# Kernel optimization log

Measured on AMD Instinct MI355X. Metric: run time of the kernel, lower is better.

The kernel has to match this reference:

```python
import jax, jax.numpy as jnp
import numpy as np

B, S, D, F, E, K = 2, 2048, 1024, 4096, 8, 2


def setup_inputs() -> dict:
    key = jax.random.key(0)
    ks = jax.random.split(key, 6)
    s = 0.02  # init scale
    return {
        "x": jax.random.normal(ks[0], (B, S, D), dtype=jnp.float32),
        "Wr": jax.random.normal(ks[1], (D, E), dtype=jnp.float32) * s,
        "br": jnp.zeros((E,), dtype=jnp.float32),
        "W1": jax.random.normal(ks[2], (E, D, F), dtype=jnp.float32) * s,
        "b1": jnp.zeros((E, F), dtype=jnp.float32),
        "W2": jax.random.normal(ks[3], (E, F, D), dtype=jnp.float32) * s,
        "b2": jnp.zeros((E, D), dtype=jnp.float32),
        "top_k": K,
    }


def reference(x, Wr, br, W1, b1, W2, b2, top_k):
    b, s, d = x.shape
    e = Wr.shape[1]
    xt = x.reshape(-1, d)                              # [T, D], T = b*s
    logits = xt @ Wr + br                              # [T, E]
    probs = jax.nn.softmax(logits, axis=-1)            # [T, E] router probabilities
    topw, topi = jax.lax.top_k(probs, top_k)           # [T, K] each
    # combine weight per (token, expert): weight if expert in token's top-k else 0
    cw = jnp.sum(jax.nn.one_hot(topi, e, dtype=x.dtype) * topw[..., None], axis=1)  # [T, E]
    # dense grouped FFN: every expert over every token, then weighted combine
    h = jax.nn.relu(jnp.einsum('td,edf->tef', xt, W1) + b1)   # [T, E, F]
    y = jnp.einsum('tef,efd->ted', h, W2) + b2                # [T, E, D]
    out = jnp.einsum('te,ted->td', cw, y).reshape(b, s, d)    # [B, S, D]
    return out, probs.reshape(b, s, e)
```

## Files before the change

kernel.cpp:

```cpp
#include <hip/hip_runtime.h>
#include <hip/hip_bf16.h>


#define T_TOK 4096
#define D_DIM 1024
#define F_DIM 4096
#define E_NUM 8
#define CAP_ROWS 9216
#define N_TILES (CAP_ROWS/128)

typedef __attribute__((ext_vector_type(8))) short short8v;
typedef __attribute__((ext_vector_type(8))) unsigned short ushort8v;
typedef __attribute__((ext_vector_type(4))) float f32x4;

static __device__ __forceinline__ unsigned short f2bf(float f){
  union { float f; unsigned u; } v; v.f = f;
  unsigned r = (v.u + 0x7fffu + ((v.u >> 16) & 1u)) >> 16;
  return (unsigned short)r;
}
static __device__ __forceinline__ float bf2f(unsigned short s){
  union { unsigned u; float f; } v; v.u = ((unsigned)s) << 16;
  return v.f;
}

static __device__ __forceinline__ void gload16(const void* g, void* l) {
  __builtin_amdgcn_global_load_lds(
      (const __attribute__((address_space(1))) unsigned int*)g,
      (__attribute__((address_space(3))) unsigned int*)l, 16, 0, 0);
}

__global__ __launch_bounds__(256) void k_init(int* counts, int* cursor,
                                              int* rows_token, float* rows_w){
  const int gid = blockIdx.x * 256 + threadIdx.x;
  if (gid < E_NUM) counts[gid] = 0;
  else if (gid < 2*E_NUM) cursor[gid - E_NUM] = 0;
  if (gid < CAP_ROWS) { rows_token[gid] = 0; rows_w[gid] = 0.f; }
}

__global__ __launch_bounds__(256) void k_router(
    const float* __restrict__ x, const float* __restrict__ Wr,
    const float* __restrict__ br, float* __restrict__ probs_out,
    int* __restrict__ topi, float* __restrict__ topw, int* __restrict__ counts)
{
  const int lane = threadIdx.x & 63;
  const int t = blockIdx.x * 4 + (threadIdx.x >> 6);
  float xv[16];
  #pragma unroll
  for (int i = 0; i < 16; ++i) xv[i] = x[(size_t)t*D_DIM + i*64 + lane];
  float pe[E_NUM];
  #pragma unroll
  for (int e = 0; e < E_NUM; ++e) {
    float p = 0.f;
    #pragma unroll
    for (int i = 0; i < 16; ++i) p += xv[i] * Wr[(i*64 + lane)*E_NUM + e];
    #pragma unroll
    for (int off = 32; off >= 1; off >>= 1) p += __shfl_xor(p, off);
    pe[e] = p + br[e];
  }
  float m = pe[0];
  #pragma unroll
  for (int e = 1; e < E_NUM; ++e) m = fmaxf(m, pe[e]);
  float s = 0.f;
  #pragma unroll
  for (int e = 0; e < E_NUM; ++e) { pe[e] = expf(pe[e] - m); s += pe[e]; }
  const float inv = 1.f / s;
  int e1 = 0; float v1 = pe[0];
  #pragma unroll
  for (int e = 1; e < E_NUM; ++e) if (pe[e] > v1) { v1 = pe[e]; e1 = e; }
  int e2 = (e1 == 0) ? 1 : 0; float v2 = pe[e2];
  #pragma unroll
  for (int e = 0; e < E_NUM; ++e) if (e != e1 && pe[e] > v2) { v2 = pe[e]; e2 = e; }
  if (lane == 0) {
    #pragma unroll
    for (int e = 0; e < E_NUM; ++e) probs_out[(size_t)t*E_NUM + e] = pe[e] * inv;
    topi[t*2+0] = e1; topw[t*2+0] = v1 * inv;
    topi[t*2+1] = e2; topw[t*2+1] = v2 * inv;
    atomicAdd(&counts[e1], 1);
    atomicAdd(&counts[e2], 1);
  }
}

__global__ void k_scan(const int* __restrict__ counts, int* __restrict__ pbase,
                       int* __restrict__ tile_e)
{
  if (threadIdx.x == 0 && blockIdx.x == 0) {
    int base = 0;
    for (int e = 0; e < E_NUM; ++e) {
      pbase[e] = base;
      const int nt = (counts[e] + 127) >> 7;
      for (int i = 0; i < nt; ++i) tile_e[(base >> 7) + i] = e;
      base += nt << 7;
    }
    pbase[E_NUM] = base;
    for (int tt = base >> 7; tt < N_TILES; ++tt) tile_e[tt] = -1;
  }
}

__global__ __launch_bounds__(256) void k_assign(
    const int* __restrict__ topi, const float* __restrict__ topw,
    const int* __restrict__ pbase, int* __restrict__ cursor,
    int* __restrict__ rows_token, float* __restrict__ rows_w,
    int* __restrict__ pair_of)
{
  const int t = blockIdx.x * 256 + threadIdx.x;
  if (t < T_TOK) {
    #pragma unroll
    for (int k = 0; k < 2; ++k) {
      const int e = topi[t*2+k];
      const int slot = atomicAdd(&cursor[e], 1);
      const int pid = pbase[e] + slot;
      rows_token[pid] = t;
      rows_w[pid] = topw[t*2+k];
      pair_of[t*2+k] = pid;
    }
  }
}

__global__ __launch_bounds__(256) void k_cvt_x(const float* __restrict__ x,
                                               unsigned short* __restrict__ xbf)
{
  const int i = (blockIdx.x * 256 + threadIdx.x) * 4;
  const float4 v = *(const float4*)&x[i];
  ushort4 o; o.x=f2bf(v.x); o.y=f2bf(v.y); o.z=f2bf(v.z); o.w=f2bf(v.w);
  *(ushort4*)&xbf[i] = o;
}

template<int R, int C>
__global__ __launch_bounds__(256) void k_tcvt(const float* __restrict__ in,
                                              unsigned short* __restrict__ out)
{
  const size_t eo = (size_t)blockIdx.z * R * C;
  const int r0 = blockIdx.y * 64, c0 = blockIdx.x * 64;
  __shared__ unsigned short ls[64][66];
  const int t = threadIdx.x;
  const int rr = t >> 4, cc = (t & 15) * 4;
  #pragma unroll
  for (int p = 0; p < 4; ++p) {
    const float4 v = *(const float4*)&in[eo + (size_t)(r0 + p*16 + rr)*C + c0 + cc];
    ls[p*16+rr][cc+0]=f2bf(v.x); ls[p*16+rr][cc+1]=f2bf(v.y);
    ls[p*16+rr][cc+2]=f2bf(v.z); ls[p*16+rr][cc+3]=f2bf(v.w);
  }
  __syncthreads();
  const int kc = (t & 7) * 8, nn0 = t >> 3;
  #pragma unroll
  for (int p = 0; p < 2; ++p) {
    const int nn = nn0 + p*32;
    ushort8v o;
    #pragma unroll
    for (int j = 0; j < 8; ++j) o[j] = ls[kc + j][nn];
    *(ushort8v*)&out[eo + (size_t)(c0 + nn)*R + r0 + kc] = o;
  }
}

template<bool GATHER, int NDIM, int KDIM, bool EPI1>
__global__ __launch_bounds__(256, 2) void k_gemm(
    const unsigned short* __restrict__ A,
    const unsigned short* __restrict__ Bt,
    const float* __restrict__ bias,
    const int* __restrict__ tile_e,
    const int* __restrict__ rows_token,
    const float* __restrict__ rows_w,
    unsigned short* __restrict__ outp)
{
  const int e = tile_e[blockIdx.y];
  if (e < 0) return;
  const int rt = blockIdx.y * 128;
  const int ntc = blockIdx.x * 128;
  __shared__ __align__(16) unsigned short LB[3][2][128*32];
  const int tid = threadIdx.x;
  const int lane = tid & 63;
  const int w = tid >> 6;
  const int seg = w & 1;
  const int isB = (w >= 2) ? 1 : 0;
  const int lrow = lane >> 2, lchunk = lane & 3;
  const unsigned short* gsrc[4];
  unsigned lds_off[4];
  if (w < 2) {
    #pragma unroll
    for (int i = 0; i < 4; ++i) {
      const int rl = seg*64 + i*16 + lrow;
      const int rowidx = GATHER ? rows_token[rt + rl] : (rt + rl);
      gsrc[i] = A + (size_t)rowidx * KDIM + lchunk*8;
      lds_off[i] = (unsigned)((seg*64 + i*16)*32);
    }
  } else {
    const unsigned short* Be = Bt + (size_t)e * NDIM * KDIM;
    #pragma unroll
    for (int i = 0; i < 4; ++i) {
      const int rl = seg*64 + i*16 + lrow;
      gsrc[i] = Be + (size_t)(ntc + rl) * KDIM + lchunk*8;
      lds_off[i] = (unsigned)((seg*64 + i*16)*32);
    }
  }
  const int wr = w >> 1, wc = w & 1;
  const int cl = lane & 15, rgb = lane >> 4;
  f32x4 acc[4][4] = {};

  constexpr int NT = KDIM / 32;
  #pragma unroll
  for (int i = 0; i < 4; ++i) gload16(gsrc[i] + 0,  &LB[0][isB][lds_off[i]]);
  #pragma unroll
  for (int i = 0; i < 4; ++i) gload16(gsrc[i] + 32, &LB[1][isB][lds_off[i]]);
  asm volatile("s_waitcnt vmcnt(4)" ::: "memory");
  __builtin_amdgcn_s_barrier();

  int buf = 0;
  for (int t = 0; t < NT; ++t) {
    const int pb = (buf == 0) ? 2 : (buf - 1);
    if (t + 2 < NT) {
      const int kof = (t + 2) * 32;
      #pragma unroll
      for (int i = 0; i < 4; ++i) gload16(gsrc[i] + kof, &LB[pb][isB][lds_off[i]]);
    }
    short8v a[4], b[4];
    #pragma unroll
    for (int m = 0; m < 4; ++m)
      a[m] = *(const short8v*)&LB[buf][0][(wr*64 + m*16 + cl)*32 + rgb*8];
    #pragma unroll
    for (int n = 0; n < 4; ++n)
      b[n] = *(const short8v*)&LB[buf][1][(wc*64 + n*16 + cl)*32 + rgb*8];
    #pragma unroll
    for (int m = 0; m < 4; ++m)
      #pragma unroll
      for (int n = 0; n < 4; ++n)
        acc[m][n] = __builtin_amdgcn_mfma_f32_16x16x32_bf16(a[m], b[n], acc[m][n], 0, 0, 0);
    if (t + 2 < NT) {
      asm volatile("s_waitcnt vmcnt(4)" ::: "memory");
    } else {
      asm volatile("s_waitcnt vmcnt(0)" ::: "memory");
    }
    __builtin_amdgcn_s_barrier();
    buf = (buf == 2) ? 0 : (buf + 1);
  }

  const size_t ebias = (size_t)e * NDIM;
  #pragma unroll
  for (int n = 0; n < 4; ++n) {
    const int col = ntc + wc*64 + n*16 + cl;
    const float bv = bias[ebias + col];
    #pragma unroll
    for (int m = 0; m < 4; ++m) {
      const int row = rt + wr*64 + m*16 + rgb*4;
      #pragma unroll
      for (int r = 0; r < 4; ++r) {
        float v = acc[m][n][r] + bv;
        if (EPI1) v = fmaxf(v, 0.f);
        else      v *= rows_w[row + r];
        const unsigned short hb = f2bf(v);
        const unsigned short ob = (unsigned short)__shfl_xor((int)(unsigned)hb, 1);
        if ((lane & 1) == 0) {
          const unsigned pk = (unsigned)hb | ((unsigned)ob << 16);
          *(unsigned*)&outp[(size_t)(row + r)*NDIM + col] = pk;
        }
      }
    }
  }
}

__global__ __launch_bounds__(256) void k_combine(
    const unsigned short* __restrict__ y, const int* __restrict__ pair_of,
    float* __restrict__ out)
{
  const int gid = blockIdx.x * 256 + threadIdx.x;
  const int t = gid >> 7;
  const int c = (gid & 127) * 8;
  const int p0 = pair_of[t*2+0];
  const int p1 = pair_of[t*2+1];
  const ushort8v a = *(const ushort8v*)&y[(size_t)p0*D_DIM + c];
  const ushort8v b = *(const ushort8v*)&y[(size_t)p1*D_DIM + c];
  float o[8];
  #pragma unroll
  for (int j = 0; j < 8; ++j) o[j] = bf2f(a[j]) + bf2f(b[j]);
  float4 o0; o0.x=o[0]; o0.y=o[1]; o0.z=o[2]; o0.w=o[3];
  float4 o1; o1.x=o[4]; o1.y=o[5]; o1.z=o[6]; o1.w=o[7];
  *(float4*)&out[(size_t)t*D_DIM + c]     = o0;
  *(float4*)&out[(size_t)t*D_DIM + c + 4] = o1;
}

extern "C" void kernel_launch(void* const* d_in, const int* in_sizes, int n_in,
                              void* d_out, int out_size, void* d_ws, size_t ws_size,
                              hipStream_t stream)
{
  const float* x  = (const float*)d_in[0];
  const float* Wr = (const float*)d_in[1];
  const float* br = (const float*)d_in[2];
  const float* W1 = (const float*)d_in[3];
  const float* b1 = (const float*)d_in[4];
  const float* W2 = (const float*)d_in[5];
  const float* b2 = (const float*)d_in[6];
  (void)in_sizes; (void)n_in; (void)out_size; (void)ws_size;

  float* out   = (float*)d_out;
  float* probs = out + (size_t)T_TOK * D_DIM;

  char* w = (char*)d_ws;
  size_t off = 0;
  int*   counts     = (int*)(w + off); off += 256;
  int*   cursor     = (int*)(w + off); off += 256;
  int*   pbase      = (int*)(w + off); off += 512;
  int*   tile_e     = (int*)(w + off); off += 3072;
  int*   topi       = (int*)(w + off); off += (size_t)T_TOK*2*4;
  float* topw       = (float*)(w + off); off += (size_t)T_TOK*2*4;
  int*   pair_of    = (int*)(w + off); off += (size_t)T_TOK*2*4;
  int*   rows_token = (int*)(w + off); off += (size_t)CAP_ROWS*4;
  float* rows_w     = (float*)(w + off); off += (size_t)CAP_ROWS*4;
  off = (off + 255) & ~(size_t)255;
  unsigned short* xbf = (unsigned short*)(w + off); off += (size_t)T_TOK*D_DIM*2;
  unsigned short* Wt  = (unsigned short*)(w + off); off += (size_t)E_NUM*D_DIM*F_DIM*2;
  unsigned short* h   = (unsigned short*)(w + off); off += (size_t)CAP_ROWS*F_DIM*2;
  unsigned short* y   = (unsigned short*)(w + off); off += (size_t)CAP_ROWS*D_DIM*2;

  k_init<<<(CAP_ROWS + 255) / 256, 256, 0, stream>>>(counts, cursor, rows_token, rows_w);
  k_router<<<T_TOK / 4, 256, 0, stream>>>(x, Wr, br, probs, topi, topw, counts);
  k_scan<<<1, 64, 0, stream>>>(counts, pbase, tile_e);
  k_assign<<<T_TOK / 256, 256, 0, stream>>>(topi, topw, pbase, cursor,
                                            rows_token, rows_w, pair_of);
  k_cvt_x<<<T_TOK * D_DIM / 4 / 256, 256, 0, stream>>>(x, xbf);
  k_tcvt<D_DIM, F_DIM><<<dim3(F_DIM/64, D_DIM/64, E_NUM), 256, 0, stream>>>(W1, Wt);
  k_gemm<true, F_DIM, D_DIM, true><<<dim3(F_DIM/128, N_TILES), 256, 0, stream>>>(
      xbf, Wt, b1, tile_e, rows_token, rows_w, h);
  k_tcvt<F_DIM, D_DIM><<<dim3(D_DIM/64, F_DIM/64, E_NUM), 256, 0, stream>>>(W2, Wt);
  k_gemm<false, D_DIM, F_DIM, false><<<dim3(D_DIM/128, N_TILES), 256, 0, stream>>>(
      h, Wt, b2, tile_e, rows_token, rows_w, y);
  k_combine<<<T_TOK * D_DIM / 8 / 256, 256, 0, stream>>>(y, pair_of, out);
}
```

Baseline: 466.5 us.

## Fuse x bf16 conversion into router, parallelize scan, remap GEMM block order

The router kernel now writes the bf16 copy of x while it already holds the values, which removes the separate conversion kernel and its extra read of x. The tile-to-expert scan now fills tile_e with many threads instead of one. Both GEMMs remap the flat block index with a stride-8 interleave, likely meant to spread tiles across the XCDs for better L2 locality. The router's bf16 stores are 2-byte scalar writes, which are less efficient than the old vectorized writes.

Result: no change. 475.2 us (+1.9%).

```diff
diff --git a/kernel.cpp b/kernel.cpp
--- a/kernel.cpp
+++ b/kernel.cpp
@@ -40,13 +40,16 @@
 __global__ __launch_bounds__(256) void k_router(
     const float* __restrict__ x, const float* __restrict__ Wr,
     const float* __restrict__ br, float* __restrict__ probs_out,
-    int* __restrict__ topi, float* __restrict__ topw, int* __restrict__ counts)
+    int* __restrict__ topi, float* __restrict__ topw, int* __restrict__ counts,
+    unsigned short* __restrict__ xbf)
 {
   const int lane = threadIdx.x & 63;
   const int t = blockIdx.x * 4 + (threadIdx.x >> 6);
   float xv[16];
   #pragma unroll
   for (int i = 0; i < 16; ++i) xv[i] = x[(size_t)t*D_DIM + i*64 + lane];
+  #pragma unroll
+  for (int i = 0; i < 16; ++i) xbf[(size_t)t*D_DIM + i*64 + lane] = f2bf(xv[i]);
   float pe[E_NUM];
   #pragma unroll
   for (int e = 0; e < E_NUM; ++e) {
@@ -80,19 +83,30 @@
   }
 }
 
-__global__ void k_scan(const int* __restrict__ counts, int* __restrict__ pbase,
-                       int* __restrict__ tile_e)
-{
-  if (threadIdx.x == 0 && blockIdx.x == 0) {
+__global__ __launch_bounds__(256) void k_scan(
+    const int* __restrict__ counts, int* __restrict__ pbase,
+    int* __restrict__ tile_e)
+{
+  __shared__ int base_s[E_NUM + 1];
+  const int tid = threadIdx.x;
+  if (tid == 0) {
     int base = 0;
+    #pragma unroll
     for (int e = 0; e < E_NUM; ++e) {
-      pbase[e] = base;
-      const int nt = (counts[e] + 127) >> 7;
-      for (int i = 0; i < nt; ++i) tile_e[(base >> 7) + i] = e;
-      base += nt << 7;
-    }
-    pbase[E_NUM] = base;
-    for (int tt = base >> 7; tt < N_TILES; ++tt) tile_e[tt] = -1;
+      base_s[e] = base;
+      base += ((counts[e] + 127) >> 7) << 7;
+    }
+    base_s[E_NUM] = base;
+  }
+  __syncthreads();
+  if (tid <= E_NUM) pbase[tid] = base_s[tid];
+  if (tid < N_TILES) {
+    const int r0 = tid << 7;
+    int e = -1;
+    #pragma unroll
+    for (int k = 0; k < E_NUM; ++k)
+      if (r0 >= base_s[k] && r0 < base_s[k+1]) e = k;
+    tile_e[tid] = e;
   }
 }
 
@@ -114,15 +128,6 @@
       pair_of[t*2+k] = pid;
     }
   }
-}
-
-__global__ __launch_bounds__(256) void k_cvt_x(const float* __restrict__ x,
-                                               unsigned short* __restrict__ xbf)
-{
-  const int i = (blockIdx.x * 256 + threadIdx.x) * 4;
-  const float4 v = *(const float4*)&x[i];
-  ushort4 o; o.x=f2bf(v.x); o.y=f2bf(v.y); o.z=f2bf(v.z); o.w=f2bf(v.w);
-  *(ushort4*)&xbf[i] = o;
 }
 
 template<int R, int C>
@@ -162,10 +167,15 @@
     const float* __restrict__ rows_w,
     unsigned short* __restrict__ outp)
 {
-  const int e = tile_e[blockIdx.y];
+  const int tot = gridDim.x * gridDim.y;
+  int flat = blockIdx.x * gridDim.y + blockIdx.y;
+  flat = (flat & 7) * (tot >> 3) + (flat >> 3);
+  const int bx = flat / gridDim.y;
+  const int by = flat % gridDim.y;
+  const int e = tile_e[by];
   if (e < 0) return;
-  const int rt = blockIdx.y * 128;
-  const int ntc = blockIdx.x * 128;
+  const int rt = by * 128;
+  const int ntc = bx * 128;
   __shared__ __align__(16) unsigned short LB[3][2][128*32];
   const int tid = threadIdx.x;
   const int lane = tid & 63;
@@ -311,11 +321,10 @@
   unsigned short* y   = (unsigned short*)(w + off); off += (size_t)CAP_ROWS*D_DIM*2;
 
   k_init<<<(CAP_ROWS + 255) / 256, 256, 0, stream>>>(counts, cursor, rows_token, rows_w);
-  k_router<<<T_TOK / 4, 256, 0, stream>>>(x, Wr, br, probs, topi, topw, counts);
-  k_scan<<<1, 64, 0, stream>>>(counts, pbase, tile_e);
+  k_router<<<T_TOK / 4, 256, 0, stream>>>(x, Wr, br, probs, topi, topw, counts, xbf);
+  k_scan<<<1, 256, 0, stream>>>(counts, pbase, tile_e);
   k_assign<<<T_TOK / 256, 256, 0, stream>>>(topi, topw, pbase, cursor,
                                             rows_token, rows_w, pair_of);
-  k_cvt_x<<<T_TOK * D_DIM / 4 / 256, 256, 0, stream>>>(x, xbf);
   k_tcvt<D_DIM, F_DIM><<<dim3(F_DIM/64, D_DIM/64, E_NUM), 256, 0, stream>>>(W1, Wt);
   k_gemm<true, F_DIM, D_DIM, true><<<dim3(F_DIM/128, N_TILES), 256, 0, stream>>>(
       xbf, Wt, b1, tile_e, rows_token, rows_w, h);
```
